# Performance work log

Measured on AMD Instinct MI355X. Metric: run time of the kernel, lower is better.

Reference implementation:

```python
import jax, jax.numpy as jnp
import numpy as np

V, E, H, T, B, L = 50000, 256, 256, 20, 64, 512
START, STOP = 18, 19
NEG = -10000.0


def setup_inputs() -> dict:
    key = jax.random.key(0)
    ks = jax.random.split(key, 16)
    lengths = jnp.sort(jax.random.randint(ks[0], (B,), 1, L + 1))[::-1]
    lengths = lengths.at[0].set(L)  # pack_padded requires sorted descending
    sentences = jax.random.randint(ks[1], (B, L), 0, V)
    s = lambda k, shp, sc: jax.random.normal(k, shp, jnp.float32) * sc
    trans = jax.random.normal(ks[12], (T, T), jnp.float32)
    trans = trans.at[START, :].set(NEG).at[:, STOP].set(NEG)
    return {
        "sentences": sentences,
        "lengths": lengths,
        "emb": s(ks[2], (V, E), 1.0),
        "w_ih_f": s(ks[3], (4 * H, E), 0.05),
        "w_hh_f": s(ks[4], (4 * H, H), 0.05),
        "b_ih_f": s(ks[5], (4 * H,), 0.05),
        "b_hh_f": s(ks[6], (4 * H,), 0.05),
        "w_ih_b": s(ks[7], (4 * H, E), 0.05),
        "w_hh_b": s(ks[8], (4 * H, H), 0.05),
        "b_ih_b": s(ks[9], (4 * H,), 0.05),
        "b_hh_b": s(ks[10], (4 * H,), 0.05),
        "w_out": s(ks[11], (T, 2 * H), 0.05),
        "b_out": s(ks[13], (T,), 0.05),
        "transitions": trans,
    }


def _lstm(x, mask, w_ih, w_hh, b_ih, b_hh):
    # x: [B,L,E]; mask: [B,L] bool. Masked scan == packed-sequence LSTM
    # (hidden frozen past length, outputs zero past length like pad_packed).
    h0 = jnp.zeros((x.shape[0], H), x.dtype)
    bias = b_ih + b_hh

    def step(carry, inp):
        h, c = carry
        xt, mt = inp
        g = xt @ w_ih.T + h @ w_hh.T + bias
        i, f, gg, o = jnp.split(g, 4, axis=-1)  # torch gate order i,f,g,o
        c_new = jax.nn.sigmoid(f) * c + jax.nn.sigmoid(i) * jnp.tanh(gg)
        h_new = jax.nn.sigmoid(o) * jnp.tanh(c_new)
        m = mt[:, None]
        h = jnp.where(m, h_new, h)
        c = jnp.where(m, c_new, c)
        return (h, c), jnp.where(m, h_new, 0.0)

    _, hs = jax.lax.scan(step, (h0, h0), (x.transpose(1, 0, 2), mask.T))
    return hs.transpose(1, 0, 2)  # [B,L,H]


def _emissions(sentences, lengths, emb, w_ih_f, w_hh_f, b_ih_f, b_hh_f,
               w_ih_b, w_hh_b, b_ih_b, b_hh_b, w_out, b_out):
    mask = jnp.arange(L)[None, :] < lengths[:, None]  # [B,L]
    embeds = emb[sentences]  # [B,L,E]
    out_f = _lstm(embeds, mask, w_ih_f, w_hh_f, b_ih_f, b_hh_f)
    # backward dir: reverse each sequence within its own length
    rev_idx = jnp.clip(lengths[:, None] - 1 - jnp.arange(L)[None, :], 0, L - 1)
    x_rev = jnp.take_along_axis(embeds, rev_idx[:, :, None], axis=1)
    h_rev = _lstm(x_rev, mask, w_ih_b, w_hh_b, b_ih_b, b_hh_b)
    out_b = jnp.take_along_axis(h_rev, rev_idx[:, :, None], axis=1) * mask[..., None]
    lstm_out = jnp.concatenate([out_f, out_b], axis=-1)  # [B,L,2H]
    return lstm_out @ w_out.T + b_out  # [B,L,T]


def _viterbi(scores, lengths, transitions):
    mask = jnp.arange(L)[None, :] < lengths[:, None]
    fv0 = jnp.full((B, T), NEG, scores.dtype).at[:, START].set(0.0)

    def step(fv, inp):
        sc_t, m_t = inp  # [B,T], [B]
        ntv = fv[:, None, :] + transitions[None]  # [B,T(next),T(prev)]
        best = jnp.argmax(ntv, axis=-1)
        fv_new = jnp.max(ntv, axis=-1) + sc_t
        fv = jnp.where(m_t[:, None], fv_new, fv)
        bp = jnp.where(m_t[:, None], best, STOP)
        return fv, bp

    fv, bps = jax.lax.scan(step, fv0, (scores.transpose(1, 0, 2), mask.T))
    terminal = fv + transitions[STOP][None, :]  # [B,T]
    last_best = jnp.argmax(terminal, axis=-1)  # [B]
    path_scores = jnp.take_along_axis(terminal, last_best[:, None], axis=1)[:, 0]

    # backtrace: j runs L-1..1; writes tag for position j-1 when j < length
    barange = jnp.arange(B)

    def back(cur, j):
        valid = j < lengths
        new = jnp.where(valid, bps[j, barange, cur], cur)
        return new, new

    js = jnp.arange(L - 1, 0, -1)
    _, tags_rev = jax.lax.scan(back, last_best, js)  # [L-1,B]
    tags = tags_rev[::-1].T  # [B,L-1], positions 0..L-2
    pos = jnp.arange(L)[None, :]
    paths = jnp.where(pos < (lengths - 1)[:, None],
                      jnp.pad(tags, ((0, 0), (0, 1))), 0)
    paths = paths.at[barange, lengths - 1].set(last_best)  # pad past length with 0
    return path_scores, paths


def reference(sentences, lengths, emb, w_ih_f, w_hh_f, b_ih_f, b_hh_f,
              w_ih_b, w_hh_b, b_ih_b, b_hh_b, w_out, b_out, transitions):
    scores = _emissions(sentences, lengths, emb, w_ih_f, w_hh_f, b_ih_f, b_hh_f,
                        w_ih_b, w_hh_b, b_ih_b, b_hh_b, w_out, b_out)
    path_scores, paths = _viterbi(scores, lengths, transitions)
    return path_scores, paths
```

## Files before the change

kernel.cpp:

```cpp
#include <hip/hip_runtime.h>
#include <hip/hip_bf16.h>
#include <math.h>

#define NV 50000
#define NE 256
#define NH 256
#define NT 20
#define NB 64
#define NL 512
#define TAG_START 18
#define TAG_STOP 19
#define NEGV -10000.0f

typedef unsigned short ushortT;
typedef __attribute__((ext_vector_type(4))) float f32x4;
typedef __attribute__((ext_vector_type(8))) short short8;

#define PINV(x) asm volatile("" : "+v"(x))

__device__ __forceinline__ float sigf_slow(float x) { return 1.0f / (1.0f + expf(-x)); }
__device__ __forceinline__ float fsig(float x) { return 1.0f / (1.0f + __expf(-x)); }
__device__ __forceinline__ float ftanh(float x) { return 1.0f - 2.0f / (1.0f + __expf(2.0f * x)); }
__device__ __forceinline__ ushortT f2bf(float f) {
    unsigned int u = __float_as_uint(f);
    u += 0x7fffu + ((u >> 16) & 1u);
    return (ushortT)(u >> 16);
}
__device__ __forceinline__ float bf2f(unsigned int bits16) {
    return __uint_as_float(bits16 << 16);
}


__global__ __launch_bounds__(256) void k_cvtw(
    const float* __restrict__ whh_f, const float* __restrict__ whh_b,
    const float* __restrict__ wih_f, const float* __restrict__ wih_b,
    ushortT* __restrict__ whh16, ushortT* __restrict__ wih16)
{
    int idx = blockIdx.x * 256 + threadIdx.x;
    const float* s; ushortT* d;
    switch (blockIdx.y) {
        case 0: s = whh_f; d = whh16;            break;
        case 1: s = whh_b; d = whh16 + 262144;   break;
        case 2: s = wih_f; d = wih16;            break;
        default: s = wih_b; d = wih16 + 262144;  break;
    }
    d[idx] = f2bf(s[idx]);
}

__global__ __launch_bounds__(1024) void k_bias(
    const float* __restrict__ bih_f, const float* __restrict__ bhh_f,
    const float* __restrict__ bih_b, const float* __restrict__ bhh_b,
    float* __restrict__ biasc)
{
    int n = threadIdx.x;
    if (blockIdx.x == 0) biasc[n] = bih_f[n] + bhh_f[n];
    else                 biasc[1024 + n] = bih_b[n] + bhh_b[n];
}

__global__
__attribute__((amdgpu_flat_work_group_size(512, 512)))
__attribute__((amdgpu_waves_per_eu(2, 2)))
void k_gin_mfma(
    const int* __restrict__ sent, const int* __restrict__ lens,
    const float* __restrict__ emb, const ushortT* __restrict__ wih16,
    const float* __restrict__ biasc, float* __restrict__ gin,
    int chunk_start, int CH)
{
    const int g = blockIdx.x, tsub = blockIdx.y;
    const int dir = blockIdx.z >> 1, half = blockIdx.z & 1;
    const int gmax = lens[g * 16];
    const int tt0 = tsub * 16;
    if (chunk_start + tt0 >= gmax) return;

    const int tid = threadIdx.x;
    const int w = tid >> 6, l = tid & 63, lr = l & 15, lg = l >> 4;

    __shared__ char x_raw[16 * 512];

    const int ucol = half * 128 + w * 16 + lr;
    short8 bfr[4][8];
    float bias_l[4];
    const ushortT* wsrc = wih16 + dir * 262144;
#pragma unroll
    for (int nt = 0; nt < 4; ++nt) {
        int col = nt * 256 + ucol;
        bias_l[nt] = biasc[dir * 1024 + col];
#pragma unroll
        for (int kt = 0; kt < 8; ++kt)
            bfr[nt][kt] = *(const short8*)(wsrc + (size_t)col * 256 + kt * 32 + lg * 8);
    }
#pragma unroll
    for (int nt = 0; nt < 4; ++nt) {
        PINV(bias_l[nt]);
#pragma unroll
        for (int kt = 0; kt < 8; ++kt) PINV(bfr[nt][kt]);
    }

    const int srow = tid >> 5, sseg = tid & 31;
    const int slen = lens[g * 16 + srow];
    const int sb = (g * 16 + srow) * 512;

    for (int i = 0; i < 16; ++i) {
        int tg = chunk_start + tt0 + i;
        if (tg >= gmax) break;

        int tsrc = dir ? (slen - 1 - tg) : tg;
        if (tsrc < 0) tsrc = 0;
        if (tsrc > 511) tsrc = 511;
        int tok = sent[sb + tsrc];
        const float* es = emb + (size_t)tok * 256 + sseg * 8;
        float4 e0 = *(const float4*)es;
        float4 e1 = *(const float4*)(es + 4);
        short8 xv;
        xv[0] = (short)f2bf(e0.x); xv[1] = (short)f2bf(e0.y);
        xv[2] = (short)f2bf(e0.z); xv[3] = (short)f2bf(e0.w);
        xv[4] = (short)f2bf(e1.x); xv[5] = (short)f2bf(e1.y);
        xv[6] = (short)f2bf(e1.z); xv[7] = (short)f2bf(e1.w);
        int sa = (srow * 512 + sseg * 16) ^ ((srow & 7) << 4);
        *(short8*)&x_raw[sa] = xv;
        __syncthreads();

        short8 af[8];
#pragma unroll
        for (int kt = 0; kt < 8; ++kt) {
            int a = (lr * 512 + kt * 64 + lg * 16) ^ ((lr & 7) << 4);
            af[kt] = *(const short8*)&x_raw[a];
        }
        f32x4 acc[4];
#pragma unroll
        for (int nt = 0; nt < 4; ++nt) {
            acc[nt][0] = bias_l[nt]; acc[nt][1] = bias_l[nt];
            acc[nt][2] = bias_l[nt]; acc[nt][3] = bias_l[nt];
        }
#pragma unroll
        for (int kt = 0; kt < 8; ++kt)
#pragma unroll
            for (int nt = 0; nt < 4; ++nt)
                acc[nt] = __builtin_amdgcn_mfma_f32_16x16x32_bf16(af[kt], bfr[nt][kt], acc[nt], 0, 0, 0);

        float* ginp = gin + ((size_t)((dir * 4 + g) * CH + (tt0 + i))) * 16384;
#pragma unroll
        for (int nt = 0; nt < 4; ++nt)
            *(f32x4*)(ginp + (nt * 256 + ucol) * 16 + lg * 4) = acc[nt];
        __syncthreads();
    }
}

__global__
__attribute__((amdgpu_flat_work_group_size(512, 512)))
__attribute__((amdgpu_waves_per_eu(2, 2)))
void k_rec_mfma(
    const int* __restrict__ lens, const ushortT* __restrict__ whh16,
    const float* __restrict__ gin, ushortT* __restrict__ hout,
    ushortT* __restrict__ st_h, float* __restrict__ st_c,
    unsigned int* __restrict__ hexu, unsigned int* __restrict__ flags,
    int chunk_start, int CH)
{
    const int g = blockIdx.x, dir = blockIdx.y, half = blockIdx.z;
    const int gmax = lens[g * 16];
    const int nsteps = min(CH, gmax - chunk_start);
    if (nsteps <= 0) return;

    const int tid = threadIdx.x;
    const int w = tid >> 6, l = tid & 63, lr = l & 15, lg = l >> 4;
    const int dirg = dir * 4 + g;

    __shared__ char h_s[2][8192];

    int lenr[4];
#pragma unroll
    for (int r = 0; r < 4; ++r) lenr[r] = lens[g * 16 + lg * 4 + r];

    const int ucol = half * 128 + w * 16 + lr;
    short8 bfr[4][8];
    {
        const ushortT* wsrc = whh16 + dir * 262144;
#pragma unroll
        for (int nt = 0; nt < 4; ++nt) {
            const ushortT* wp = wsrc + (size_t)(nt * 256 + ucol) * 256 + lg * 8;
#pragma unroll
            for (int kt = 0; kt < 8; ++kt)
                bfr[nt][kt] = *(const short8*)(wp + kt * 32);
        }
    }

    float c[4];
    if (chunk_start == 0) {
#pragma unroll
        for (int r = 0; r < 4; ++r) c[r] = 0.0f;
        for (int i = tid; i < 2048; i += 512) ((int*)h_s[0])[i] = 0;
    } else {
        const float* cs = st_c + ((size_t)(dirg * 2 + half)) * 2048 + tid * 4;
#pragma unroll
        for (int r = 0; r < 4; ++r) c[r] = cs[r];
        const int* hs = (const int*)st_h + dirg * 2048;
        for (int i = tid; i < 2048; i += 512) ((int*)h_s[0])[i] = hs[i];
    }
    __syncthreads();

    unsigned int* exu = hexu + dirg * 4096;
    unsigned int* flagMe = flags + dirg * 2 + half;
    unsigned int* flagPeer = flags + dirg * 2 + (half ^ 1);

    const int pub_base = ucol * 8 + lg * 2;

    int pf_uidx[2], pf_lds0[2], pf_lds1[2];
#pragma unroll
    for (int s2 = 0; s2 < 2; ++s2) {
        int i = tid * 2 + s2;
        int pcol = ((half ^ 1) << 7) + (i >> 3);
        int sub = i & 7;
        pf_uidx[s2] = pcol * 8 + sub;
        int r0 = (sub >> 1) * 4 + (sub & 1) * 2;
        pf_lds0[s2] = (r0 * 512 + pcol * 2) ^ ((r0 & 7) << 4);
        int r1 = r0 + 1;
        pf_lds1[s2] = (r1 * 512 + pcol * 2) ^ ((r1 & 7) << 4);
    }

    const float* ginp = gin + (size_t)dirg * CH * 16384;
    int p = 0;
    for (int tt = 0; tt < nsteps; ++tt) {
        const int t_glob = chunk_start + tt;

        f32x4 gv[4];
#pragma unroll
        for (int nt = 0; nt < 4; ++nt)
            gv[nt] = *(const f32x4*)(ginp + (size_t)tt * 16384 + (nt * 256 + ucol) * 16 + lg * 4);

        const char* hb = h_s[p];
        f32x4 acc[4];
#pragma unroll
        for (int nt = 0; nt < 4; ++nt) { acc[nt][0] = 0.f; acc[nt][1] = 0.f; acc[nt][2] = 0.f; acc[nt][3] = 0.f; }
#pragma unroll
        for (int kt = 0; kt < 8; ++kt) {
            int a_ = (lr * 512 + kt * 64 + lg * 16) ^ ((lr & 7) << 4);
            short8 af = *(const short8*)&hb[a_];
#pragma unroll
            for (int nt = 0; nt < 4; ++nt)
                acc[nt] = __builtin_amdgcn_mfma_f32_16x16x32_bf16(af, bfr[nt][kt], acc[nt], 0, 0, 0);
        }

        char* hw = h_s[p ^ 1];
        unsigned int* exs = exu + ((t_glob + 1) & 1) * 2048;
        ushortT hh[4];
#pragma unroll
        for (int r = 0; r < 4; ++r) {
            float i_ = acc[0][r] + gv[0][r];
            float f_ = acc[1][r] + gv[1][r];
            float g_ = acc[2][r] + gv[2][r];
            float o_ = acc[3][r] + gv[3][r];
            float cn = fsig(f_) * c[r] + fsig(i_) * ftanh(g_);
            float hn = fsig(o_) * ftanh(cn);
            c[r] = cn;
            hh[r] = f2bf(hn);
            int row = lg * 4 + r;
            *(ushortT*)&hw[(row * 512 + ucol * 2) ^ ((row & 7) << 4)] = hh[r];
        }
        unsigned int v01 = (unsigned int)hh[0] | ((unsigned int)hh[1] << 16);
        unsigned int v23 = (unsigned int)hh[2] | ((unsigned int)hh[3] << 16);
        __hip_atomic_store(&exs[pub_base + 0], v01, __ATOMIC_RELAXED, __HIP_MEMORY_SCOPE_AGENT);
        __hip_atomic_store(&exs[pub_base + 1], v23, __ATOMIC_RELAXED, __HIP_MEMORY_SCOPE_AGENT);
#pragma unroll
        for (int r = 0; r < 4; ++r) {
            if (t_glob < lenr[r]) {
                int row = lg * 4 + r;
                int tp = dir ? (lenr[r] - 1 - t_glob) : t_glob;
                hout[((size_t)((g * 16 + row) * 512 + tp)) * 512 + dir * 256 + ucol] = hh[r];
            }
        }

        __syncthreads();

        if (tid == 0)
            __hip_atomic_store(flagMe, (unsigned int)(t_glob + 1), __ATOMIC_RELEASE, __HIP_MEMORY_SCOPE_AGENT);

        {
            unsigned int tgt = (unsigned int)(t_glob + 1);
            int guard = 0;
            while (__hip_atomic_load(flagPeer, __ATOMIC_RELAXED, __HIP_MEMORY_SCOPE_AGENT) < tgt
                   && ++guard < (1 << 16)) {}
        }

#pragma unroll
        for (int s2 = 0; s2 < 2; ++s2) {
            unsigned int v = __hip_atomic_load(&exs[pf_uidx[s2]], __ATOMIC_RELAXED, __HIP_MEMORY_SCOPE_AGENT);
            *(ushortT*)&hw[pf_lds0[s2]] = (ushortT)(v & 0xffffu);
            *(ushortT*)&hw[pf_lds1[s2]] = (ushortT)(v >> 16);
        }
        __syncthreads();
        p ^= 1;
    }

    float* cs = st_c + ((size_t)(dirg * 2 + half)) * 2048 + tid * 4;
#pragma unroll
    for (int r = 0; r < 4; ++r) cs[r] = c[r];
    if (half == 0) {
        int* hs = (int*)st_h + dirg * 2048;
        for (int i = tid; i < 2048; i += 512) hs[i] = ((int*)h_s[p])[i];
    }
}

__global__ __launch_bounds__(256) void k_scores_bf(
    const int* __restrict__ lens, const ushortT* __restrict__ hout,
    const float* __restrict__ w_out, const float* __restrict__ b_out,
    float* __restrict__ scores)
{
    const int b = blockIdx.y;
    const int t0 = blockIdx.x * 32;
    const int len = lens[b];
    if (t0 >= len) return;

    __shared__ float w_s[20 * 513];
    __shared__ float row_s[512];
    __shared__ float part_s[20][9];
    __shared__ float bo_s[20];

    const int tid = threadIdx.x;
    for (int e = tid; e < 20 * 512; e += 256) w_s[(e >> 9) * 513 + (e & 511)] = w_out[e];
    if (tid < 20) bo_s[tid] = b_out[tid];
    __syncthreads();

    const int tend = min(t0 + 32, len);
    const int tag = tid >> 3, sl = tid & 7;
    for (int t = t0; t < tend; ++t) {
        const ushortT* hr = hout + ((size_t)(b * 512 + t)) * 512;
        unsigned int v = ((const unsigned int*)hr)[tid];
        row_s[tid * 2] = bf2f(v & 0xffffu);
        row_s[tid * 2 + 1] = bf2f(v >> 16);
        __syncthreads();
        if (tid < 160) {
            float s = 0.0f;
#pragma unroll 8
            for (int j = 0; j < 64; ++j) {
                int k = sl + (((j + tag) & 63) << 3);
                s = fmaf(w_s[tag * 513 + k], row_s[k], s);
            }
            part_s[tag][sl] = s;
        }
        __syncthreads();
        if (tid < 20) {
            float s = bo_s[tid];
#pragma unroll
            for (int j = 0; j < 8; ++j) s += part_s[tid][j];
            scores[((size_t)(b * 512 + t)) * 20 + tid] = s;
        }
        __syncthreads();
    }
}

__global__ __launch_bounds__(64) void k_viterbi_s(
    const int* __restrict__ lens, const float* __restrict__ scores,
    const float* __restrict__ trans, float* __restrict__ out)
{
    const int b = blockIdx.x;
    const int lane = threadIdx.x;
    const int len = lens[b];

    __shared__ float tr_s[20][21];
    __shared__ float fv_s[20];
    __shared__ float term_s[20];
    __shared__ unsigned char bp_s[512][20];
    __shared__ unsigned char path_s[512];

    for (int e = lane; e < 400; e += 64) tr_s[e / 20][e % 20] = trans[e];
    if (lane < 20) fv_s[lane] = (lane == TAG_START) ? 0.0f : NEGV;
    __syncthreads();

    const float* sc = scores + ((size_t)(b << 9)) * 20;
    for (int t = 0; t < len; ++t) {
        float m = 0.0f; int arg = 0;
        if (lane < 20) {
            m = fv_s[0] + tr_s[lane][0]; arg = 0;
#pragma unroll
            for (int k = 1; k < 20; ++k) {
                float v = fv_s[k] + tr_s[lane][k];
                if (v > m) { m = v; arg = k; }
            }
            m += sc[t * 20 + lane];
        }
        __syncthreads();
        if (lane < 20) { fv_s[lane] = m; bp_s[t][lane] = (unsigned char)arg; }
        __syncthreads();
    }

    if (lane < 20) term_s[lane] = fv_s[lane] + tr_s[TAG_STOP][lane];
    __syncthreads();

    if (lane == 0) {
        float m = term_s[0]; int arg = 0;
        for (int k = 1; k < 20; ++k) if (term_s[k] > m) { m = term_s[k]; arg = k; }
        out[b] = m;
        int cur = arg;
        path_s[len - 1] = (unsigned char)cur;
        for (int j = len - 1; j >= 1; --j) {
            cur = bp_s[j][cur];
            path_s[j - 1] = (unsigned char)cur;
        }
    }
    __syncthreads();

    float* po = out + NB + ((size_t)b << 9);
    for (int p = lane; p < NL; p += 64) po[p] = (p < len) ? (float)path_s[p] : 0.0f;
}

__global__ __launch_bounds__(256) void k_transpose_fb(
    const float* __restrict__ whh_f, const float* __restrict__ whh_b,
    const float* __restrict__ wih_f, const float* __restrict__ wih_b,
    float* __restrict__ thh_f, float* __restrict__ thh_b,
    float* __restrict__ tih_f, float* __restrict__ tih_b)
{
    int e = blockIdx.x * 256 + threadIdx.x;
    const float* wm; float* wt;
    switch (blockIdx.y) {
        case 0: wm = whh_f; wt = thh_f; break;
        case 1: wm = whh_b; wt = thh_b; break;
        case 2: wm = wih_f; wt = tih_f; break;
        default: wm = wih_b; wt = tih_b; break;
    }
    int n = e >> 8, k = e & 255;
    wt[k * 1024 + n] = wm[e];
}

__global__ __launch_bounds__(1024) void k_rec_fb(
    const int* __restrict__ sent, const int* __restrict__ lens,
    const float* __restrict__ emb,
    const float* __restrict__ thh_f, const float* __restrict__ thh_b,
    const float* __restrict__ tih_f, const float* __restrict__ tih_b,
    const float* __restrict__ b_ih_f, const float* __restrict__ b_hh_f,
    const float* __restrict__ b_ih_b, const float* __restrict__ b_hh_b,
    const float* __restrict__ w_out,
    float* __restrict__ sc_f, float* __restrict__ sc_b)
{
    const int b = blockIdx.x, dir = blockIdx.y;
    const int len = lens[b];
    const int n = threadIdx.x;
    const float* Whh = dir ? thh_b : thh_f;
    const float* Wih = dir ? tih_b : tih_f;
    const float* bi = dir ? b_ih_b : b_ih_f;
    const float* bh = dir ? b_hh_b : b_hh_f;
    float* scout = dir ? sc_b : sc_f;

    __shared__ float x_s[256];
    __shared__ float h_s[256];
    __shared__ float g_s[1024];
    __shared__ float bias_s[1024];
    __shared__ float wout_s[20 * 257];
    __shared__ float part_s[20][8];

    bias_s[n] = bi[n] + bh[n];
    for (int e = n; e < 20 * 256; e += 1024)
        wout_s[(e >> 8) * 257 + (e & 255)] = w_out[(e >> 8) * 512 + dir * 256 + (e & 255)];
    if (n < 256) h_s[n] = 0.0f;
    float c = 0.0f;
    __syncthreads();

    const int sbase = b << 9;
    for (int t = 0; t < len; ++t) {
        if (n < 256) {
            int ti = dir ? (len - 1 - t) : t;
            int tok = sent[sbase + ti];
            x_s[n] = emb[(size_t)tok * NE + n];
        }
        __syncthreads();
        float acc = bias_s[n];
        const float* wi = Wih + n;
        const float* wh = Whh + n;
#pragma unroll 8
        for (int k = 0; k < 256; ++k) {
            acc = fmaf(wh[(size_t)(k << 10)], h_s[k], acc);
            acc = fmaf(wi[(size_t)(k << 10)], x_s[k], acc);
        }
        g_s[n] = acc;
        __syncthreads();
        if (n < 256) {
            float ig = g_s[n], fg = g_s[n + 256], gg = g_s[n + 512], og = g_s[n + 768];
            float cn = sigf_slow(fg) * c + sigf_slow(ig) * tanhf(gg);
            float hn = sigf_slow(og) * tanhf(cn);
            c = cn; h_s[n] = hn;
        }
        __syncthreads();
        if (n < 160) {
            const int tag = n >> 3, sl = n & 7;
            const float* wrow = wout_s + tag * 257;
            float s = 0.0f;
#pragma unroll 8
            for (int j = 0; j < 32; ++j) { int k = sl + (j << 3); s = fmaf(wrow[k], h_s[k], s); }
            part_s[tag][sl] = s;
        }
        __syncthreads();
        if (n < 20) {
            float s = part_s[n][0];
#pragma unroll
            for (int j = 1; j < 8; ++j) s += part_s[n][j];
            int tp = dir ? (len - 1 - t) : t;
            scout[(size_t)(sbase + tp) * 20 + n] = s;
        }
    }
}

__global__ __launch_bounds__(64) void k_viterbi_fb(
    const int* __restrict__ lens,
    const float* __restrict__ sc_f, const float* __restrict__ sc_b,
    const float* __restrict__ b_out, const float* __restrict__ trans,
    float* __restrict__ out)
{
    const int b = blockIdx.x;
    const int lane = threadIdx.x;
    const int len = lens[b];

    __shared__ float tr_s[20][21];
    __shared__ float fv_s[20];
    __shared__ float term_s[20];
    __shared__ float bo_s[20];
    __shared__ unsigned char bp_s[512][20];
    __shared__ unsigned char path_s[512];

    for (int e = lane; e < 400; e += 64) tr_s[e / 20][e % 20] = trans[e];
    if (lane < 20) { fv_s[lane] = (lane == TAG_START) ? 0.0f : NEGV; bo_s[lane] = b_out[lane]; }
    __syncthreads();

    const size_t sb = (size_t)(b << 9) * 20;
    for (int t = 0; t < len; ++t) {
        float m = 0.0f; int arg = 0;
        if (lane < 20) {
            m = fv_s[0] + tr_s[lane][0]; arg = 0;
#pragma unroll
            for (int k = 1; k < 20; ++k) {
                float v = fv_s[k] + tr_s[lane][k];
                if (v > m) { m = v; arg = k; }
            }
            m += sc_f[sb + t * 20 + lane] + sc_b[sb + t * 20 + lane] + bo_s[lane];
        }
        __syncthreads();
        if (lane < 20) { fv_s[lane] = m; bp_s[t][lane] = (unsigned char)arg; }
        __syncthreads();
    }
    if (lane < 20) term_s[lane] = fv_s[lane] + tr_s[TAG_STOP][lane];
    __syncthreads();
    if (lane == 0) {
        float m = term_s[0]; int arg = 0;
        for (int k = 1; k < 20; ++k) if (term_s[k] > m) { m = term_s[k]; arg = k; }
        out[b] = m;
        int cur = arg;
        path_s[len - 1] = (unsigned char)cur;
        for (int j = len - 1; j >= 1; --j) { cur = bp_s[j][cur]; path_s[j - 1] = (unsigned char)cur; }
    }
    __syncthreads();
    float* po = out + NB + ((size_t)b << 9);
    for (int p = lane; p < NL; p += 64) po[p] = (p < len) ? (float)path_s[p] : 0.0f;
}

extern "C" void kernel_launch(void* const* d_in, const int* in_sizes, int n_in,
                              void* d_out, int out_size, void* d_ws, size_t ws_size,
                              hipStream_t stream)
{
    const int*   sent   = (const int*)d_in[0];
    const int*   lens   = (const int*)d_in[1];
    const float* emb    = (const float*)d_in[2];
    const float* w_ih_f = (const float*)d_in[3];
    const float* w_hh_f = (const float*)d_in[4];
    const float* b_ih_f = (const float*)d_in[5];
    const float* b_hh_f = (const float*)d_in[6];
    const float* w_ih_b = (const float*)d_in[7];
    const float* w_hh_b = (const float*)d_in[8];
    const float* b_ih_b = (const float*)d_in[9];
    const float* b_hh_b = (const float*)d_in[10];
    const float* w_out  = (const float*)d_in[11];
    const float* b_out  = (const float*)d_in[12];
    const float* trans  = (const float*)d_in[13];
    float* out = (float*)d_out;

    char* w = (char*)d_ws;
    const size_t base = 38612992;
    int CH = 0;
    const int chs[6] = {512, 256, 192, 128, 64, 32};
    for (int i = 0; i < 6; ++i)
        if (base + (size_t)chs[i] * 524288 <= ws_size) { CH = chs[i]; break; }

    if (CH) {
        ushortT* whh16 = (ushortT*)(w);
        ushortT* wih16 = (ushortT*)(w + 1048576);
        float*   biasc = (float*)(w + 2097152);
        ushortT* st_h  = (ushortT*)(w + 2105344);
        float*   st_c  = (float*)(w + 2170880);
        unsigned int* hexu = (unsigned int*)(w + 2301952);
        unsigned int* flags = (unsigned int*)(w + 2433024);
        float*   scores= (float*)(w + 2437120);
        ushortT* hout  = (ushortT*)(w + 5058560);
        float*   gin   = (float*)(w + base);

        hipMemsetAsync(flags, 0, 4096, stream);
        k_cvtw<<<dim3(1024, 4), 256, 0, stream>>>(w_hh_f, w_hh_b, w_ih_f, w_ih_b, whh16, wih16);
        k_bias<<<2, 1024, 0, stream>>>(b_ih_f, b_hh_f, b_ih_b, b_hh_b, biasc);

        for (int cs = 0; cs < NL; cs += CH) {
            k_gin_mfma<<<dim3(4, CH / 16, 4), 512, 0, stream>>>(
                sent, lens, emb, wih16, biasc, gin, cs, CH);
            k_rec_mfma<<<dim3(4, 2, 2), 512, 0, stream>>>(
                lens, whh16, gin, hout, st_h, st_c, hexu, flags, cs, CH);
        }
        k_scores_bf<<<dim3(16, 64), 256, 0, stream>>>(lens, hout, w_out, b_out, scores);
        k_viterbi_s<<<64, 64, 0, stream>>>(lens, scores, trans, out);
    } else {
        float* ws2   = (float*)d_ws;
        float* thh_f = ws2;
        float* thh_b = thh_f + 262144;
        float* tih_f = thh_b + 262144;
        float* tih_b = tih_f + 262144;
        float* sc_f  = tih_b + 262144;
        float* sc_b  = sc_f + (size_t)NB * NL * NT;

        k_transpose_fb<<<dim3(1024, 4), 256, 0, stream>>>(
            w_hh_f, w_hh_b, w_ih_f, w_ih_b, thh_f, thh_b, tih_f, tih_b);
        k_rec_fb<<<dim3(NB, 2), 1024, 0, stream>>>(
            sent, lens, emb, thh_f, thh_b, tih_f, tih_b,
            b_ih_f, b_hh_f, b_ih_b, b_hh_b, w_out, sc_f, sc_b);
        k_viterbi_fb<<<NB, 64, 0, stream>>>(lens, sc_f, sc_b, b_out, trans, out);
    }
}
```

Baseline: 2.400 ms.

## Merge recurrent half-blocks into one workgroup, pin weights in AGPRs, store gates as bf16

Previously each direction/group's recurrence was split across two workgroups that exchanged h every timestep through global memory with flag spin-waits. Now a single workgroup computes all 256 hidden units, which removes that cross-block exchange. Half of W_hh (the i and f gates) is kept in AGPRs through inline asm, and the g and o gate weights are re-read from global/L2 every step. The precomputed input gates are stored as bf16 to halve their traffic, at the cost of precision and of doubled per-block MFMA work on the serial critical path.

```diff
diff --git a/kernel.cpp b/kernel.cpp
--- a/kernel.cpp
+++ b/kernel.cpp
@@ -15,6 +15,7 @@
 typedef unsigned short ushortT;
 typedef __attribute__((ext_vector_type(4))) float f32x4;
 typedef __attribute__((ext_vector_type(8))) short short8;
+typedef __attribute__((ext_vector_type(4))) unsigned short us4;
 
 #define PINV(x) asm volatile("" : "+v"(x))
 
@@ -30,6 +31,40 @@
     return __uint_as_float(bits16 << 16);
 }
 
+#define WRW(A0,A1,A2,A3,PTR) do {                                   \
+    int4 _u = *(const int4*)(PTR);                                  \
+    asm volatile("v_accvgpr_write_b32 a" #A0 ", %0\n\t"             \
+                 "v_accvgpr_write_b32 a" #A1 ", %1\n\t"             \
+                 "v_accvgpr_write_b32 a" #A2 ", %2\n\t"             \
+                 "v_accvgpr_write_b32 a" #A3 ", %3"                 \
+                 :: "v"(_u.x), "v"(_u.y), "v"(_u.z), "v"(_u.w)      \
+                 : "a" #A0, "a" #A1, "a" #A2, "a" #A3);             \
+} while (0)
+
+#define MFMA_AG(ACC, AF, A0,A1,A2,A3)                                           \
+    asm volatile("v_mfma_f32_16x16x32_bf16 %0, %1, a[" #A0 ":" #A3 "], %0"      \
+                 : "+v"(ACC) : "v"(AF) : "a" #A0, "a" #A1, "a" #A2, "a" #A3)
+
+#define MFMA_SV(ACC, AF, BW)                                                    \
+    asm volatile("v_mfma_f32_16x16x32_bf16 %0, %1, %2, %0"                      \
+                 : "+v"(ACC) : "v"(AF), "v"(BW))
+
+#define KT_BLOCK(KT, I0a,I0b,I0c,I0d, I1a,I1b,I1c,I1d, F0a,F0b,F0c,F0d, F1a,F1b,F1c,F1d) \
+    {                                                                                     \
+        int a_ = (lr * 512 + (KT) * 64 + lg * 16) ^ ((lr & 7) << 4);                      \
+        short8 af = *(const short8*)&hb[a_];                                              \
+        MFMA_AG(acc0, af, I0a,I0b,I0c,I0d);                                               \
+        MFMA_AG(acc1, af, I1a,I1b,I1c,I1d);                                               \
+        MFMA_AG(acc2, af, F0a,F0b,F0c,F0d);                                               \
+        MFMA_AG(acc3, af, F1a,F1b,F1c,F1d);                                               \
+        MFMA_SV(acc4, af, wg0[KT]);                                                       \
+        MFMA_SV(acc5, af, wg1[KT]);                                                       \
+        MFMA_SV(acc6, af, wo0[KT]);                                                       \
+        MFMA_SV(acc7, af, wo1[KT]);                                                       \
+    }
+
+#define BARRIER_LGKM() asm volatile("s_waitcnt lgkmcnt(0)\n\ts_barrier" ::: "memory")
+
 
 __global__ __launch_bounds__(256) void k_cvtw(
     const float* __restrict__ whh_f, const float* __restrict__ whh_b,
@@ -63,7 +98,7 @@
 void k_gin_mfma(
     const int* __restrict__ sent, const int* __restrict__ lens,
     const float* __restrict__ emb, const ushortT* __restrict__ wih16,
-    const float* __restrict__ biasc, float* __restrict__ gin,
+    const float* __restrict__ biasc, ushortT* __restrict__ gin16,
     int chunk_start, int CH)
 {
     const int g = blockIdx.x, tsub = blockIdx.y;
@@ -138,10 +173,15 @@
             for (int nt = 0; nt < 4; ++nt)
                 acc[nt] = __builtin_amdgcn_mfma_f32_16x16x32_bf16(af[kt], bfr[nt][kt], acc[nt], 0, 0, 0);
 
-        float* ginp = gin + ((size_t)((dir * 4 + g) * CH + (tt0 + i))) * 16384;
-#pragma unroll
-        for (int nt = 0; nt < 4; ++nt)
-            *(f32x4*)(ginp + (nt * 256 + ucol) * 16 + lg * 4) = acc[nt];
+        ushortT* gp = gin16 + ((size_t)((dir * 4 + g) * CH + (tt0 + i))) * 16384;
+#pragma unroll
+        for (int nt = 0; nt < 4; ++nt) {
+            int col = nt * 256 + ucol;
+            us4 st;
+            st[0] = f2bf(acc[nt][0]); st[1] = f2bf(acc[nt][1]);
+            st[2] = f2bf(acc[nt][2]); st[3] = f2bf(acc[nt][3]);
+            *(us4*)(gp + col * 16 + lg * 4) = st;
+        }
         __syncthreads();
     }
 }
@@ -151,12 +191,11 @@
 __attribute__((amdgpu_waves_per_eu(2, 2)))
 void k_rec_mfma(
     const int* __restrict__ lens, const ushortT* __restrict__ whh16,
-    const float* __restrict__ gin, ushortT* __restrict__ hout,
+    const ushortT* __restrict__ gin16, ushortT* __restrict__ hout,
     ushortT* __restrict__ st_h, float* __restrict__ st_c,
-    unsigned int* __restrict__ hexu, unsigned int* __restrict__ flags,
     int chunk_start, int CH)
 {
-    const int g = blockIdx.x, dir = blockIdx.y, half = blockIdx.z;
+    const int g = blockIdx.x, dir = blockIdx.y;
     const int gmax = lens[g * 16];
     const int nsteps = min(CH, gmax - chunk_start);
     if (nsteps <= 0) return;
@@ -171,133 +210,149 @@
 #pragma unroll
     for (int r = 0; r < 4; ++r) lenr[r] = lens[g * 16 + lg * 4 + r];
 
-    const int ucol = half * 128 + w * 16 + lr;
-    short8 bfr[4][8];
+    const ushortT* wsrc = whh16 + dir * 262144;
+    const int u0 = w * 32 + lr, u1 = w * 32 + 16 + lr;
+
     {
-        const ushortT* wsrc = whh16 + dir * 262144;
-#pragma unroll
-        for (int nt = 0; nt < 4; ++nt) {
-            const ushortT* wp = wsrc + (size_t)(nt * 256 + ucol) * 256 + lg * 8;
-#pragma unroll
-            for (int kt = 0; kt < 8; ++kt)
-                bfr[nt][kt] = *(const short8*)(wp + kt * 32);
-        }
-    }
-
-    float c[4];
+        const ushortT* qi0 = wsrc + (size_t)(0   + u0) * 256 + lg * 8;
+        const ushortT* qi1 = wsrc + (size_t)(0   + u1) * 256 + lg * 8;
+        const ushortT* qf0 = wsrc + (size_t)(256 + u0) * 256 + lg * 8;
+        const ushortT* qf1 = wsrc + (size_t)(256 + u1) * 256 + lg * 8;
+        WRW(  0,  1,  2,  3, qi0 +   0); WRW(  4,  5,  6,  7, qi0 +  32);
+        WRW(  8,  9, 10, 11, qi0 +  64); WRW( 12, 13, 14, 15, qi0 +  96);
+        WRW( 16, 17, 18, 19, qi0 + 128); WRW( 20, 21, 22, 23, qi0 + 160);
+        WRW( 24, 25, 26, 27, qi0 + 192); WRW( 28, 29, 30, 31, qi0 + 224);
+        WRW( 32, 33, 34, 35, qi1 +   0); WRW( 36, 37, 38, 39, qi1 +  32);
+        WRW( 40, 41, 42, 43, qi1 +  64); WRW( 44, 45, 46, 47, qi1 +  96);
+        WRW( 48, 49, 50, 51, qi1 + 128); WRW( 52, 53, 54, 55, qi1 + 160);
+        WRW( 56, 57, 58, 59, qi1 + 192); WRW( 60, 61, 62, 63, qi1 + 224);
+        WRW( 64, 65, 66, 67, qf0 +   0); WRW( 68, 69, 70, 71, qf0 +  32);
+        WRW( 72, 73, 74, 75, qf0 +  64); WRW( 76, 77, 78, 79, qf0 +  96);
+        WRW( 80, 81, 82, 83, qf0 + 128); WRW( 84, 85, 86, 87, qf0 + 160);
+        WRW( 88, 89, 90, 91, qf0 + 192); WRW( 92, 93, 94, 95, qf0 + 224);
+        WRW( 96, 97, 98, 99, qf1 +   0); WRW(100,101,102,103, qf1 +  32);
+        WRW(104,105,106,107, qf1 +  64); WRW(108,109,110,111, qf1 +  96);
+        WRW(112,113,114,115, qf1 + 128); WRW(116,117,118,119, qf1 + 160);
+        WRW(120,121,122,123, qf1 + 192); WRW(124,125,126,127, qf1 + 224);
+        asm volatile("s_nop 1");
+    }
+
+    const ushortT* pg0 = wsrc + (size_t)(512 + u0) * 256 + lg * 8;
+    const ushortT* pg1 = wsrc + (size_t)(512 + u1) * 256 + lg * 8;
+    const ushortT* po0 = wsrc + (size_t)(768 + u0) * 256 + lg * 8;
+    const ushortT* po1 = wsrc + (size_t)(768 + u1) * 256 + lg * 8;
+
+    float c[2][4];
     if (chunk_start == 0) {
 #pragma unroll
-        for (int r = 0; r < 4; ++r) c[r] = 0.0f;
+        for (int s = 0; s < 2; ++s)
+#pragma unroll
+            for (int r = 0; r < 4; ++r) c[s][r] = 0.0f;
         for (int i = tid; i < 2048; i += 512) ((int*)h_s[0])[i] = 0;
     } else {
-        const float* cs = st_c + ((size_t)(dirg * 2 + half)) * 2048 + tid * 4;
-#pragma unroll
-        for (int r = 0; r < 4; ++r) c[r] = cs[r];
+        const float* cs = st_c + ((size_t)dirg * 512 + tid) * 8;
+#pragma unroll
+        for (int s = 0; s < 2; ++s)
+#pragma unroll
+            for (int r = 0; r < 4; ++r) c[s][r] = cs[s * 4 + r];
         const int* hs = (const int*)st_h + dirg * 2048;
         for (int i = tid; i < 2048; i += 512) ((int*)h_s[0])[i] = hs[i];
     }
     __syncthreads();
 
-    unsigned int* exu = hexu + dirg * 4096;
-    unsigned int* flagMe = flags + dirg * 2 + half;
-    unsigned int* flagPeer = flags + dirg * 2 + (half ^ 1);
-
-    const int pub_base = ucol * 8 + lg * 2;
-
-    int pf_uidx[2], pf_lds0[2], pf_lds1[2];
-#pragma unroll
-    for (int s2 = 0; s2 < 2; ++s2) {
-        int i = tid * 2 + s2;
-        int pcol = ((half ^ 1) << 7) + (i >> 3);
-        int sub = i & 7;
-        pf_uidx[s2] = pcol * 8 + sub;
-        int r0 = (sub >> 1) * 4 + (sub & 1) * 2;
-        pf_lds0[s2] = (r0 * 512 + pcol * 2) ^ ((r0 & 7) << 4);
-        int r1 = r0 + 1;
-        pf_lds1[s2] = (r1 * 512 + pcol * 2) ^ ((r1 & 7) << 4);
-    }
-
-    const float* ginp = gin + (size_t)dirg * CH * 16384;
+    const ushortT* ginp = gin16 + (size_t)dirg * CH * 16384;
+
     int p = 0;
     for (int tt = 0; tt < nsteps; ++tt) {
         const int t_glob = chunk_start + tt;
 
-        f32x4 gv[4];
-#pragma unroll
-        for (int nt = 0; nt < 4; ++nt)
-            gv[nt] = *(const f32x4*)(ginp + (size_t)tt * 16384 + (nt * 256 + ucol) * 16 + lg * 4);
+        const ushortT* gb = ginp + (size_t)tt * 16384 + lg * 4;
+        us4 gvi0 = *(const us4*)(gb + (0   + u0) * 16);
+        us4 gvi1 = *(const us4*)(gb + (0   + u1) * 16);
+        us4 gvf0 = *(const us4*)(gb + (256 + u0) * 16);
+        us4 gvf1 = *(const us4*)(gb + (256 + u1) * 16);
+        us4 gvg0 = *(const us4*)(gb + (512 + u0) * 16);
+        us4 gvg1 = *(const us4*)(gb + (512 + u1) * 16);
+        us4 gvo0 = *(const us4*)(gb + (768 + u0) * 16);
+        us4 gvo1 = *(const us4*)(gb + (768 + u1) * 16);
+
+        short8 wg0[8], wg1[8], wo0[8], wo1[8];
+#pragma unroll
+        for (int kt = 0; kt < 8; ++kt) {
+            wg0[kt] = *(const short8*)(pg0 + kt * 32);
+            wg1[kt] = *(const short8*)(pg1 + kt * 32);
+            wo0[kt] = *(const short8*)(po0 + kt * 32);
+            wo1[kt] = *(const short8*)(po1 + kt * 32);
+        }
 
         const char* hb = h_s[p];
-        f32x4 acc[4];
-#pragma unroll
-        for (int nt = 0; nt < 4; ++nt) { acc[nt][0] = 0.f; acc[nt][1] = 0.f; acc[nt][2] = 0.f; acc[nt][3] = 0.f; }
-#pragma unroll
-        for (int kt = 0; kt < 8; ++kt) {
-            int a_ = (lr * 512 + kt * 64 + lg * 16) ^ ((lr & 7) << 4);
-            short8 af = *(const short8*)&hb[a_];
-#pragma unroll
-            for (int nt = 0; nt < 4; ++nt)
-                acc[nt] = __builtin_amdgcn_mfma_f32_16x16x32_bf16(af, bfr[nt][kt], acc[nt], 0, 0, 0);
-        }
+        f32x4 acc0 = {0.f,0.f,0.f,0.f}, acc1 = {0.f,0.f,0.f,0.f};
+        f32x4 acc2 = {0.f,0.f,0.f,0.f}, acc3 = {0.f,0.f,0.f,0.f};
+        f32x4 acc4 = {0.f,0.f,0.f,0.f}, acc5 = {0.f,0.f,0.f,0.f};
+        f32x4 acc6 = {0.f,0.f,0.f,0.f}, acc7 = {0.f,0.f,0.f,0.f};
+
+        KT_BLOCK(0,   0,  1,  2,  3,  32, 33, 34, 35,  64, 65, 66, 67,  96, 97, 98, 99)
+        KT_BLOCK(1,   4,  5,  6,  7,  36, 37, 38, 39,  68, 69, 70, 71, 100,101,102,103)
+        KT_BLOCK(2,   8,  9, 10, 11,  40, 41, 42, 43,  72, 73, 74, 75, 104,105,106,107)
+        KT_BLOCK(3,  12, 13, 14, 15,  44, 45, 46, 47,  76, 77, 78, 79, 108,109,110,111)
+        KT_BLOCK(4,  16, 17, 18, 19,  48, 49, 50, 51,  80, 81, 82, 83, 112,113,114,115)
+        KT_BLOCK(5,  20, 21, 22, 23,  52, 53, 54, 55,  84, 85, 86, 87, 116,117,118,119)
+        KT_BLOCK(6,  24, 25, 26, 27,  56, 57, 58, 59,  88, 89, 90, 91, 120,121,122,123)
+        KT_BLOCK(7,  28, 29, 30, 31,  60, 61, 62, 63,  92, 93, 94, 95, 124,125,126,127)
+
+        asm volatile("s_nop 7\n\ts_nop 7");
 
         char* hw = h_s[p ^ 1];
-        unsigned int* exs = exu + ((t_glob + 1) & 1) * 2048;
-        ushortT hh[4];
+        ushortT hh0[4], hh1[4];
 #pragma unroll
         for (int r = 0; r < 4; ++r) {
-            float i_ = acc[0][r] + gv[0][r];
-            float f_ = acc[1][r] + gv[1][r];
-            float g_ = acc[2][r] + gv[2][r];
-            float o_ = acc[3][r] + gv[3][r];
-            float cn = fsig(f_) * c[r] + fsig(i_) * ftanh(g_);
+            float i_ = acc0[r] + bf2f(gvi0[r]);
+            float f_ = acc2[r] + bf2f(gvf0[r]);
+            float g_ = acc4[r] + bf2f(gvg0[r]);
+            float o_ = acc6[r] + bf2f(gvo0[r]);
+            float cn = fsig(f_) * c[0][r] + fsig(i_) * ftanh(g_);
             float hn = fsig(o_) * ftanh(cn);
-            c[r] = cn;
-            hh[r] = f2bf(hn);
+            c[0][r] = cn;
+            hh0[r] = f2bf(hn);
             int row = lg * 4 + r;
-            *(ushortT*)&hw[(row * 512 + ucol * 2) ^ ((row & 7) << 4)] = hh[r];
-        }
-        unsigned int v01 = (unsigned int)hh[0] | ((unsigned int)hh[1] << 16);
-        unsigned int v23 = (unsigned int)hh[2] | ((unsigned int)hh[3] << 16);
-        __hip_atomic_store(&exs[pub_base + 0], v01, __ATOMIC_RELAXED, __HIP_MEMORY_SCOPE_AGENT);
-        __hip_atomic_store(&exs[pub_base + 1], v23, __ATOMIC_RELAXED, __HIP_MEMORY_SCOPE_AGENT);
+            *(ushortT*)&hw[(row * 512 + u0 * 2) ^ ((row & 7) << 4)] = hh0[r];
+        }
+#pragma unroll
+        for (int r = 0; r < 4; ++r) {
+            float i_ = acc1[r] + bf2f(gvi1[r]);
+            float f_ = acc3[r] + bf2f(gvf1[r]);
+            float g_ = acc5[r] + bf2f(gvg1[r]);
+            float o_ = acc7[r] + bf2f(gvo1[r]);
+            float cn = fsig(f_) * c[1][r] + fsig(i_) * ftanh(g_);
+            float hn = fsig(o_) * ftanh(cn);
+            c[1][r] = cn;
+            hh1[r] = f2bf(hn);
+            int row = lg * 4 + r;
+            *(ushortT*)&hw[(row * 512 + u1 * 2) ^ ((row & 7) << 4)] = hh1[r];
+        }
+
 #pragma unroll
         for (int r = 0; r < 4; ++r) {
             if (t_glob < lenr[r]) {
                 int row = lg * 4 + r;
                 int tp = dir ? (lenr[r] - 1 - t_glob) : t_glob;
-                hout[((size_t)((g * 16 + row) * 512 + tp)) * 512 + dir * 256 + ucol] = hh[r];
+                size_t base = ((size_t)((g * 16 + row) * 512 + tp)) * 512 + dir * 256;
+                hout[base + u0] = hh0[r];
+                hout[base + u1] = hh1[r];
             }
         }
 
-        __syncthreads();
-
-        if (tid == 0)
-            __hip_atomic_store(flagMe, (unsigned int)(t_glob + 1), __ATOMIC_RELEASE, __HIP_MEMORY_SCOPE_AGENT);
-
-        {
-            unsigned int tgt = (unsigned int)(t_glob + 1);
-            int guard = 0;
-            while (__hip_atomic_load(flagPeer, __ATOMIC_RELAXED, __HIP_MEMORY_SCOPE_AGENT) < tgt
-                   && ++guard < (1 << 16)) {}
-        }
-
-#pragma unroll
-        for (int s2 = 0; s2 < 2; ++s2) {
-            unsigned int v = __hip_atomic_load(&exs[pf_uidx[s2]], __ATOMIC_RELAXED, __HIP_MEMORY_SCOPE_AGENT);
-            *(ushortT*)&hw[pf_lds0[s2]] = (ushortT)(v & 0xffffu);
-            *(ushortT*)&hw[pf_lds1[s2]] = (ushortT)(v >> 16);
-        }
-        __syncthreads();
+        BARRIER_LGKM();
         p ^= 1;
     }
 
-    float* cs = st_c + ((size_t)(dirg * 2 + half)) * 2048 + tid * 4;
-#pragma unroll
-    for (int r = 0; r < 4; ++r) cs[r] = c[r];
-    if (half == 0) {
-        int* hs = (int*)st_h + dirg * 2048;
-        for (int i = tid; i < 2048; i += 512) hs[i] = ((int*)h_s[p])[i];
-    }
+    float* cs = st_c + ((size_t)dirg * 512 + tid) * 8;
+#pragma unroll
+    for (int s = 0; s < 2; ++s)
+#pragma unroll
+        for (int r = 0; r < 4; ++r) cs[s * 4 + r] = c[s][r];
+    int* hs = (int*)st_h + dirg * 2048;
+    for (int i = tid; i < 2048; i += 512) hs[i] = ((int*)h_s[p])[i];
 }
 
 __global__ __launch_bounds__(256) void k_scores_bf(
@@ -575,7 +630,7 @@
     int CH = 0;
     const int chs[6] = {512, 256, 192, 128, 64, 32};
     for (int i = 0; i < 6; ++i)
-        if (base + (size_t)chs[i] * 524288 <= ws_size) { CH = chs[i]; break; }
+        if (base + (size_t)chs[i] * 262144 <= ws_size) { CH = chs[i]; break; }
 
     if (CH) {
         ushortT* whh16 = (ushortT*)(w);
@@ -583,21 +638,18 @@
         float*   biasc = (float*)(w + 2097152);
         ushortT* st_h  = (ushortT*)(w + 2105344);
         float*   st_c  = (float*)(w + 2170880);
-        unsigned int* hexu = (unsigned int*)(w + 2301952);
-        unsigned int* flags = (unsigned int*)(w + 2433024);
         float*   scores= (float*)(w + 2437120);
         ushortT* hout  = (ushortT*)(w + 5058560);
-        float*   gin   = (float*)(w + base);
-
-        hipMemsetAsync(flags, 0, 4096, stream);
+        ushortT* gin16 = (ushortT*)(w + base);
+
         k_cvtw<<<dim3(1024, 4), 256, 0, stream>>>(w_hh_f, w_hh_b, w_ih_f, w_ih_b, whh16, wih16);
         k_bias<<<2, 1024, 0, stream>>>(b_ih_f, b_hh_f, b_ih_b, b_hh_b, biasc);
 
         for (int cs = 0; cs < NL; cs += CH) {
             k_gin_mfma<<<dim3(4, CH / 16, 4), 512, 0, stream>>>(
-                sent, lens, emb, wih16, biasc, gin, cs, CH);
-            k_rec_mfma<<<dim3(4, 2, 2), 512, 0, stream>>>(
-                lens, whh16, gin, hout, st_h, st_c, hexu, flags, cs, CH);
+                sent, lens, emb, wih16, biasc, gin16, cs, CH);
+            k_rec_mfma<<<dim3(4, 2), 512, 0, stream>>>(
+                lens, whh16, gin16, hout, st_h, st_c, cs, CH);
         }
         k_scores_bf<<<dim3(16, 64), 256, 0, stream>>>(lens, hout, w_out, b_out, scores);
         k_viterbi_s<<<64, 64, 0, stream>>>(lens, scores, trans, out);
```

After: 5.561 ms. 132% more time.
